# Performance work log

Hardware: AMD Instinct MI355X
Metric: run time of the kernel (lower is better)

## Reference

```python
import jax, jax.numpy as jnp
import numpy as np

B, LQ, LK, D = 16, 2048, 2048, 64
TEMPERATURE = 8.0  # sqrt(d_k)


def setup_inputs() -> dict:
    key = jax.random.key(0)
    kq, kk, kv, km = jax.random.split(key, 4)
    q = jax.random.normal(kq, (B, LQ, D), dtype=jnp.float32)
    k = jax.random.normal(kk, (B, LK, D), dtype=jnp.float32)
    v = jax.random.normal(kv, (B, LK, D), dtype=jnp.float32)
    mask = jax.random.randint(km, (B, LQ, LK), 0, 2).astype(jnp.bool_)
    return {"q": q, "k": k, "v": v, "mask": mask}


def reference(q, k, v, mask):
    # attn = bmm(q, k^T) / temperature  -> [B, LQ, LK]
    attn = jnp.einsum("bqd,bkd->bqk", q, k) / TEMPERATURE
    attn = jnp.where(mask, -jnp.inf, attn)
    attn = jax.nn.softmax(attn, axis=2)
    out = jnp.einsum("bqk,bkd->bqd", attn, v)  # [B, LQ, D]
    return out, attn
```

## Files before the change

### kernel.cpp

```cpp
#include <hip/hip_runtime.h>
#include <hip/hip_bf16.h>

namespace {
constexpr int kB = 16;
constexpr int kLQ = 2048;
constexpr int kLK = 2048;
constexpr int kD = 64;
constexpr float kLog2e = 1.44269504088896340736f;
constexpr int kQT = 64;
constexpr int kKT = 512;
constexpr int kKStrB = 144;
constexpr int kMStrB = 40;
constexpr int kBStrB = 72;
constexpr int kChunk = 256;
constexpr int kEStrB = 528;
}

using short8 = __attribute__((ext_vector_type(8))) short;
using f32x4 = __attribute__((ext_vector_type(4))) float;

union S8U { short8 v; unsigned u[4]; };

static __device__ __forceinline__ unsigned pk2(float lo, float hi) {
    __hip_bfloat162 h = __float22bfloat162_rn(float2{lo, hi});
    unsigned short a = __builtin_bit_cast(unsigned short, h.x);
    unsigned short b = __builtin_bit_cast(unsigned short, h.y);
    return (unsigned)a | ((unsigned)b << 16);
}
static __device__ __forceinline__ float bf2f(unsigned short s) {
    unsigned u = ((unsigned)s) << 16;
    return __builtin_bit_cast(float, u);
}

__global__ __launch_bounds__(256, 8) void k1_qke(
    const float* __restrict__ qg, const float* __restrict__ kg,
    const void* __restrict__ maskg, unsigned short* __restrict__ ews,
    float* __restrict__ outg)
{
    __shared__ __align__(16) unsigned char s_kst[32 * kKStrB];
    __shared__ __align__(16) unsigned char s_mst[64 * kMStrB];
    __shared__ __align__(16) unsigned char s_bnc[4][16 * kBStrB];
    __shared__ int s_flag;

    const int tid = threadIdx.x;
    const int wave = tid >> 6;
    const int lane = tid & 63;
    const int r16 = lane & 15;
    const int g = lane >> 4;

    const int blk = blockIdx.x;
    const int b = blk >> 7;
    const int kt = (blk >> 5) & 3;
    const int qt = blk & 31;
    const int rows0 = qt * kQT;
    const int c0 = kt * kKT;

    if (tid < 64) {
        unsigned w = ((const unsigned*)maskg)[tid];
        unsigned long long bal = __ballot((w & 0xFFFFFF00u) != 0u);
        if (tid == 0) s_flag = (bal != 0ull) ? 1 : 0;
    }
    __syncthreads();
    const bool mask_byte = (s_flag != 0);
    const unsigned char* mask_u8 = (const unsigned char*)maskg;
    const int* mask_i32 = (const int*)maskg;

    short8 q0, q1;
    {
        const float4* qp = (const float4*)(qg + ((size_t)b * kLQ + rows0 + wave * 16 + r16) * kD);
        const float s = 0.125f * kLog2e;
        float4 x0 = qp[2*g + 0], x1 = qp[2*g + 1];
        float4 x2 = qp[2*g + 8], x3 = qp[2*g + 9];
        x0 *= s; x1 *= s; x2 *= s; x3 *= s;
        S8U a, c;
        a.u[0] = pk2(x0.x, x0.y); a.u[1] = pk2(x0.z, x0.w);
        a.u[2] = pk2(x1.x, x1.y); a.u[3] = pk2(x1.z, x1.w);
        c.u[0] = pk2(x2.x, x2.y); c.u[1] = pk2(x2.z, x2.w);
        c.u[2] = pk2(x3.x, x3.y); c.u[3] = pk2(x3.z, x3.w);
        q0 = a.v; q1 = c.v;
    }

    float wsum = 0.f;

    for (int sub = 0; sub < kKT / 32; ++sub) {
        const int csub = c0 + sub * 32;
        {
            const int krow = tid >> 3;
            const int d8 = (tid & 7) * 8;
            const float4* kp = (const float4*)(kg + ((size_t)b * kLK + csub + krow) * kD + d8);
            float4 y0 = kp[0], y1 = kp[1];
            S8U p;
            p.u[0] = pk2(y0.x, y0.y); p.u[1] = pk2(y0.z, y0.w);
            p.u[2] = pk2(y1.x, y1.y); p.u[3] = pk2(y1.z, y1.w);
            *(short8*)(s_kst + krow * kKStrB + d8 * 2) = p.v;
        }
        {
            const int mrow = tid >> 2;
            const int mc = (tid & 3) * 8;
            unsigned long long f;
            if (mask_byte) {
                f = *(const unsigned long long*)(mask_u8 +
                        ((size_t)b * kLQ + rows0 + mrow) * (size_t)kLK + csub + mc);
            } else {
                const int* mp = mask_i32 + ((size_t)b * kLQ + rows0 + mrow) * (size_t)kLK + csub + mc;
                const int4 m0 = *(const int4*)mp;
                const int4 m1 = *(const int4*)(mp + 4);
                f  = (m0.x ? 1ull : 0ull)       | (m0.y ? 1ull << 8 : 0ull)
                   | (m0.z ? 1ull << 16 : 0ull) | (m0.w ? 1ull << 24 : 0ull)
                   | (m1.x ? 1ull << 32 : 0ull) | (m1.y ? 1ull << 40 : 0ull)
                   | (m1.z ? 1ull << 48 : 0ull) | (m1.w ? 1ull << 56 : 0ull);
            }
            *(unsigned long long*)(s_mst + mrow * kMStrB + mc) = f;
        }
        __syncthreads();

        const short8 kA0 = *(const short8*)(s_kst + r16 * kKStrB + g * 16);
        const short8 kA1 = *(const short8*)(s_kst + r16 * kKStrB + 64 + g * 16);
        const short8 kB0 = *(const short8*)(s_kst + (16 + r16) * kKStrB + g * 16);
        const short8 kB1 = *(const short8*)(s_kst + (16 + r16) * kKStrB + 64 + g * 16);
        f32x4 accA = {0.f, 0.f, 0.f, 0.f}, accB = {0.f, 0.f, 0.f, 0.f};
        accA = __builtin_amdgcn_mfma_f32_16x16x32_bf16(kA0, q0, accA, 0, 0, 0);
        accA = __builtin_amdgcn_mfma_f32_16x16x32_bf16(kA1, q1, accA, 0, 0, 0);
        accB = __builtin_amdgcn_mfma_f32_16x16x32_bf16(kB0, q0, accB, 0, 0, 0);
        accB = __builtin_amdgcn_mfma_f32_16x16x32_bf16(kB1, q1, accB, 0, 0, 0);

        const unsigned mwA = *(const unsigned*)(s_mst + (wave * 16 + r16) * kMStrB + 4 * g);
        const unsigned mwB = *(const unsigned*)(s_mst + (wave * 16 + r16) * kMStrB + 16 + 4 * g);
        float eA[4], eB[4];
#pragma unroll
        for (int r = 0; r < 4; ++r) {
            eA[r] = ((mwA >> (8*r)) & 0xFFu) ? 0.f : __builtin_amdgcn_exp2f(accA[r]);
            eB[r] = ((mwB >> (8*r)) & 0xFFu) ? 0.f : __builtin_amdgcn_exp2f(accB[r]);
        }
        wsum += (eA[0] + eA[1]) + (eA[2] + eA[3]) + (eB[0] + eB[1]) + (eB[2] + eB[3]);
        uint2 pA{ pk2(eA[0], eA[1]), pk2(eA[2], eA[3]) };
        uint2 pB{ pk2(eB[0], eB[1]), pk2(eB[2], eB[3]) };
        *(uint2*)(s_bnc[wave] + r16 * kBStrB + 8 * g) = pA;
        *(uint2*)(s_bnc[wave] + r16 * kBStrB + 32 + 8 * g) = pB;
        __syncthreads();

        {
            const int row = tid >> 2;
            const int seg = tid & 3;
            const S8U* src = (const S8U*)(s_bnc[row >> 4] + (row & 15) * kBStrB + seg * 16);
            unsigned short* dst = ews + ((size_t)b * kLQ + rows0 + row) * (size_t)kLK + csub + seg * 8;
            *(short8*)dst = src->v;
        }
    }
    wsum += __shfl_xor(wsum, 16, 64);
    wsum += __shfl_xor(wsum, 32, 64);
    if (g == 0)
        outg[((size_t)b * kLQ + rows0 + wave * 16 + r16) * kD + kt] = wsum;
}

__global__ __launch_bounds__(512, 8) void k2_norm_pv(
    const float* __restrict__ vg, const unsigned short* __restrict__ ews,
    float* __restrict__ attng, float* __restrict__ outg)
{
    __shared__ __align__(16) unsigned char s_e[16 * kEStrB];
    __shared__ float s_red[16][kD];
    __shared__ float s_rinv[16];

    const int tid = threadIdx.x;
    const int wave = tid >> 6;
    const int lane = tid & 63;
    const int r16 = lane & 15;
    const int g = lane >> 4;

    const int blk = blockIdx.x;
    const int b = blk >> 7;
    const int row0 = (blk & 127) * 16;

    if (tid < 64) {
        const int r = tid >> 2, p = tid & 3;
        float ps = outg[((size_t)b * kLQ + row0 + r) * kD + p];
        ps += __shfl_xor(ps, 1, 64);
        ps += __shfl_xor(ps, 2, 64);
        if (p == 0) s_rinv[r] = __builtin_amdgcn_rcpf(ps);
    }
    __syncthreads();

    const int d0 = (wave & 3) * 16;
    const int kh = wave >> 2;
    f32x4 acc = {0.f, 0.f, 0.f, 0.f};
    const float* vbase = vg + (size_t)b * kLK * kD + d0 + r16;

    for (int chunk = 0; chunk < kLK / kChunk; ++chunk) {
        const int c0 = chunk * kChunk;
        {
            const int row = tid >> 5;
            const int cc = tid & 31;
            const float rinv = s_rinv[row];
            const unsigned short* ep = ews + ((size_t)b * kLQ + row0 + row) * (size_t)kLK + c0 + cc * 8;
            const short8 ev = *(const short8*)ep;
            *(short8*)(s_e + row * kEStrB + cc * 16) = ev;
            float* ap = attng + ((size_t)b * kLQ + row0 + row) * (size_t)kLK + c0 + cc * 8;
            f32x4 a0, a1;
            a0[0] = bf2f((unsigned short)ev[0]) * rinv;
            a0[1] = bf2f((unsigned short)ev[1]) * rinv;
            a0[2] = bf2f((unsigned short)ev[2]) * rinv;
            a0[3] = bf2f((unsigned short)ev[3]) * rinv;
            a1[0] = bf2f((unsigned short)ev[4]) * rinv;
            a1[1] = bf2f((unsigned short)ev[5]) * rinv;
            a1[2] = bf2f((unsigned short)ev[6]) * rinv;
            a1[3] = bf2f((unsigned short)ev[7]) * rinv;
            *(f32x4*)ap = a0;
            *(f32x4*)(ap + 4) = a1;
        }
        __syncthreads();
#pragma unroll
        for (int s = 0; s < 4; ++s) {
            const int kk = kh * 128 + s * 32 + 8 * g;
            const short8 af = *(const short8*)(s_e + r16 * kEStrB + kk * 2);
            const float* vp = vbase + (size_t)(c0 + kk) * kD;
            float v0 = vp[0*kD], v1 = vp[1*kD], v2 = vp[2*kD], v3 = vp[3*kD];
            float v4 = vp[4*kD], v5 = vp[5*kD], v6 = vp[6*kD], v7 = vp[7*kD];
            S8U bv;
            bv.u[0] = pk2(v0, v1); bv.u[1] = pk2(v2, v3);
            bv.u[2] = pk2(v4, v5); bv.u[3] = pk2(v6, v7);
            acc = __builtin_amdgcn_mfma_f32_16x16x32_bf16(af, bv.v, acc, 0, 0, 0);
        }
        __syncthreads();
    }

    if (kh == 1) {
#pragma unroll
        for (int r = 0; r < 4; ++r) s_red[4*g + r][d0 + r16] = acc[r];
    }
    __syncthreads();
    if (kh == 0) {
#pragma unroll
        for (int r = 0; r < 4; ++r) {
            const int m = 4*g + r;
            outg[((size_t)b * kLQ + row0 + m) * kD + d0 + r16] =
                (acc[r] + s_red[m][d0 + r16]) * s_rinv[m];
        }
    }
}

extern "C" void kernel_launch(void* const* d_in, const int* in_sizes, int n_in,
                              void* d_out, int out_size, void* d_ws, size_t ws_size,
                              hipStream_t stream) {
    (void)in_sizes; (void)n_in; (void)out_size; (void)ws_size;
    const float* q = (const float*)d_in[0];
    const float* k = (const float*)d_in[1];
    const float* v = (const float*)d_in[2];
    const void* mask = d_in[3];
    float* out = (float*)d_out;
    float* attn = out + (size_t)kB * kLQ * kD;
    unsigned short* ews = (unsigned short*)d_ws;
    k1_qke<<<dim3(kB * 128), 256, 0, stream>>>(q, k, mask, ews, out);
    k2_norm_pv<<<dim3(kB * 128), 512, 0, stream>>>(v, ews, attn, out);
}
```

Baseline: 284.2 us.

## Give each k1 block full key rows and move attn normalization into k1

The first kernel now assigns each block 16 query rows across the full key length, with 128-key sub-tiles split across four waves. This lets the block compute complete row sums itself and write the normalized fp32 attention matrix, which previously happened in the second kernel. The second kernel is reduced to the P·V product using the stored reciprocal. The cost is that K is reloaded and converted by 128 blocks per batch instead of 32, and the exp workspace is read back right after being written (likely from L2). Occupancy also drops because the launch bound goes from 8 to 6 and LDS use is larger.

After: 288.3 us. About the same (+1.4%).

```diff
diff --git a/kernel.cpp b/kernel.cpp
--- a/kernel.cpp
+++ b/kernel.cpp
@@ -7,17 +7,15 @@
 constexpr int kLK = 2048;
 constexpr int kD = 64;
 constexpr float kLog2e = 1.44269504088896340736f;
-constexpr int kQT = 64;
-constexpr int kKT = 512;
 constexpr int kKStrB = 144;
-constexpr int kMStrB = 40;
-constexpr int kBStrB = 72;
+constexpr int kMStrB = 136;
+constexpr int kBStrB = 272;
 constexpr int kChunk = 256;
 constexpr int kEStrB = 528;
 }
 
 using short8 = __attribute__((ext_vector_type(8))) short;
-using f32x4 = __attribute__((ext_vector_type(4))) float;
+using f32x4  = __attribute__((ext_vector_type(4))) float;
 
 union S8U { short8 v; unsigned u[4]; };
 
@@ -32,14 +30,16 @@
     return __builtin_bit_cast(float, u);
 }
 
-__global__ __launch_bounds__(256, 8) void k1_qke(
+__global__ __launch_bounds__(256, 6) void k1_fused(
     const float* __restrict__ qg, const float* __restrict__ kg,
     const void* __restrict__ maskg, unsigned short* __restrict__ ews,
-    float* __restrict__ outg)
+    float* __restrict__ attng, float* __restrict__ outg)
 {
-    __shared__ __align__(16) unsigned char s_kst[32 * kKStrB];
-    __shared__ __align__(16) unsigned char s_mst[64 * kMStrB];
-    __shared__ __align__(16) unsigned char s_bnc[4][16 * kBStrB];
+    __shared__ __align__(16) unsigned char s_kst[128 * kKStrB];
+    __shared__ __align__(16) unsigned char s_mst[16 * kMStrB];
+    __shared__ __align__(16) unsigned char s_bnc[16 * kBStrB];
+    __shared__ float s_wsum[4][16];
+    __shared__ float s_rinv[16];
     __shared__ int s_flag;
 
     const int tid = threadIdx.x;
@@ -50,10 +50,8 @@
 
     const int blk = blockIdx.x;
     const int b = blk >> 7;
-    const int kt = (blk >> 5) & 3;
-    const int qt = blk & 31;
-    const int rows0 = qt * kQT;
-    const int c0 = kt * kKT;
+    const int qt = blk & 127;
+    const size_t grow0 = (size_t)b * kLQ + qt * 16;
 
     if (tid < 64) {
         unsigned w = ((const unsigned*)maskg)[tid];
@@ -67,7 +65,7 @@
 
     short8 q0, q1;
     {
-        const float4* qp = (const float4*)(qg + ((size_t)b * kLQ + rows0 + wave * 16 + r16) * kD);
+        const float4* qp = (const float4*)(qg + (grow0 + r16) * kD);
         const float s = 0.125f * kLog2e;
         float4 x0 = qp[2*g + 0], x1 = qp[2*g + 1];
         float4 x2 = qp[2*g + 8], x3 = qp[2*g + 9];
@@ -82,50 +80,47 @@
 
     float wsum = 0.f;
 
-    for (int sub = 0; sub < kKT / 32; ++sub) {
-        const int csub = c0 + sub * 32;
+    for (int sub = 0; sub < kLK / 128; ++sub) {
+        const int csub = sub * 128;
+#pragma unroll
+        for (int i = 0; i < 8; ++i) {
+            const int row = (tid >> 4) + i * 16;
+            const float4 y = *(const float4*)(kg + ((size_t)b * kLK + csub + row) * kD + (tid & 15) * 4);
+            uint2 p{ pk2(y.x, y.y), pk2(y.z, y.w) };
+            *(uint2*)(s_kst + row * kKStrB + (tid & 15) * 8) = p;
+        }
         {
-            const int krow = tid >> 3;
-            const int d8 = (tid & 7) * 8;
-            const float4* kp = (const float4*)(kg + ((size_t)b * kLK + csub + krow) * kD + d8);
-            float4 y0 = kp[0], y1 = kp[1];
-            S8U p;
-            p.u[0] = pk2(y0.x, y0.y); p.u[1] = pk2(y0.z, y0.w);
-            p.u[2] = pk2(y1.x, y1.y); p.u[3] = pk2(y1.z, y1.w);
-            *(short8*)(s_kst + krow * kKStrB + d8 * 2) = p.v;
-        }
-        {
-            const int mrow = tid >> 2;
-            const int mc = (tid & 3) * 8;
+            const int mrow = tid >> 4;
+            const int mseg = tid & 15;
             unsigned long long f;
             if (mask_byte) {
-                f = *(const unsigned long long*)(mask_u8 +
-                        ((size_t)b * kLQ + rows0 + mrow) * (size_t)kLK + csub + mc);
+                f = *(const unsigned long long*)(mask_u8 + (grow0 + mrow) * kLK + csub + mseg * 8);
             } else {
-                const int* mp = mask_i32 + ((size_t)b * kLQ + rows0 + mrow) * (size_t)kLK + csub + mc;
+                const int* mp = mask_i32 + (grow0 + mrow) * kLK + csub + mseg * 8;
                 const int4 m0 = *(const int4*)mp;
                 const int4 m1 = *(const int4*)(mp + 4);
-                f  = (m0.x ? 1ull : 0ull)       | (m0.y ? 1ull << 8 : 0ull)
-                   | (m0.z ? 1ull << 16 : 0ull) | (m0.w ? 1ull << 24 : 0ull)
-                   | (m1.x ? 1ull << 32 : 0ull) | (m1.y ? 1ull << 40 : 0ull)
-                   | (m1.z ? 1ull << 48 : 0ull) | (m1.w ? 1ull << 56 : 0ull);
+                f  = (m0.x ? 1ull : 0ull)        | (m0.y ? 1ull << 8 : 0ull)
+                   | (m0.z ? 1ull << 16 : 0ull)  | (m0.w ? 1ull << 24 : 0ull)
+                   | (m1.x ? 1ull << 32 : 0ull)  | (m1.y ? 1ull << 40 : 0ull)
+                   | (m1.z ? 1ull << 48 : 0ull)  | (m1.w ? 1ull << 56 : 0ull);
             }
-            *(unsigned long long*)(s_mst + mrow * kMStrB + mc) = f;
-        }
-        __syncthreads();
-
-        const short8 kA0 = *(const short8*)(s_kst + r16 * kKStrB + g * 16);
-        const short8 kA1 = *(const short8*)(s_kst + r16 * kKStrB + 64 + g * 16);
-        const short8 kB0 = *(const short8*)(s_kst + (16 + r16) * kKStrB + g * 16);
-        const short8 kB1 = *(const short8*)(s_kst + (16 + r16) * kKStrB + 64 + g * 16);
+            *(unsigned long long*)(s_mst + mrow * kMStrB + mseg * 8) = f;
+        }
+        __syncthreads();
+
+        const unsigned char* kb = s_kst + (wave * 32 + r16) * kKStrB;
+        const short8 kA0 = *(const short8*)(kb + g * 16);
+        const short8 kA1 = *(const short8*)(kb + 64 + g * 16);
+        const short8 kB0 = *(const short8*)(kb + 16 * kKStrB + g * 16);
+        const short8 kB1 = *(const short8*)(kb + 16 * kKStrB + 64 + g * 16);
         f32x4 accA = {0.f, 0.f, 0.f, 0.f}, accB = {0.f, 0.f, 0.f, 0.f};
         accA = __builtin_amdgcn_mfma_f32_16x16x32_bf16(kA0, q0, accA, 0, 0, 0);
         accA = __builtin_amdgcn_mfma_f32_16x16x32_bf16(kA1, q1, accA, 0, 0, 0);
         accB = __builtin_amdgcn_mfma_f32_16x16x32_bf16(kB0, q0, accB, 0, 0, 0);
         accB = __builtin_amdgcn_mfma_f32_16x16x32_bf16(kB1, q1, accB, 0, 0, 0);
 
-        const unsigned mwA = *(const unsigned*)(s_mst + (wave * 16 + r16) * kMStrB + 4 * g);
-        const unsigned mwB = *(const unsigned*)(s_mst + (wave * 16 + r16) * kMStrB + 16 + 4 * g);
+        const unsigned mwA = *(const unsigned*)(s_mst + r16 * kMStrB + wave * 32 + 4 * g);
+        const unsigned mwB = *(const unsigned*)(s_mst + r16 * kMStrB + wave * 32 + 16 + 4 * g);
         float eA[4], eB[4];
 #pragma unroll
         for (int r = 0; r < 4; ++r) {
@@ -135,27 +130,51 @@
         wsum += (eA[0] + eA[1]) + (eA[2] + eA[3]) + (eB[0] + eB[1]) + (eB[2] + eB[3]);
         uint2 pA{ pk2(eA[0], eA[1]), pk2(eA[2], eA[3]) };
         uint2 pB{ pk2(eB[0], eB[1]), pk2(eB[2], eB[3]) };
-        *(uint2*)(s_bnc[wave] + r16 * kBStrB + 8 * g) = pA;
-        *(uint2*)(s_bnc[wave] + r16 * kBStrB + 32 + 8 * g) = pB;
+        *(uint2*)(s_bnc + r16 * kBStrB + wave * 64 + 8 * g) = pA;
+        *(uint2*)(s_bnc + r16 * kBStrB + wave * 64 + 32 + 8 * g) = pB;
         __syncthreads();
 
         {
-            const int row = tid >> 2;
-            const int seg = tid & 3;
-            const S8U* src = (const S8U*)(s_bnc[row >> 4] + (row & 15) * kBStrB + seg * 16);
-            unsigned short* dst = ews + ((size_t)b * kLQ + rows0 + row) * (size_t)kLK + csub + seg * 8;
-            *(short8*)dst = src->v;
-        }
-    }
+            const int erow = tid >> 4;
+            const int eseg = tid & 15;
+            *(short8*)(ews + (grow0 + erow) * kLK + csub + eseg * 8) =
+                *(const short8*)(s_bnc + erow * kBStrB + eseg * 16);
+        }
+    }
+
     wsum += __shfl_xor(wsum, 16, 64);
     wsum += __shfl_xor(wsum, 32, 64);
-    if (g == 0)
-        outg[((size_t)b * kLQ + rows0 + wave * 16 + r16) * kD + kt] = wsum;
-}
-
-__global__ __launch_bounds__(512, 8) void k2_norm_pv(
+    if (g == 0) s_wsum[wave][r16] = wsum;
+    __syncthreads();
+    if (tid < 16) {
+        const float rs = s_wsum[0][tid] + s_wsum[1][tid] + s_wsum[2][tid] + s_wsum[3][tid];
+        outg[(grow0 + tid) * kD] = rs;
+        s_rinv[tid] = __builtin_amdgcn_rcpf(rs);
+    }
+    __syncthreads();
+
+#pragma unroll 2
+    for (int r = 0; r < 16; ++r) {
+        const float rinv = s_rinv[r];
+        const short8 ev = *(const short8*)(ews + (grow0 + r) * kLK + tid * 8);
+        f32x4 a0, a1;
+        a0[0] = bf2f((unsigned short)ev[0]) * rinv;
+        a0[1] = bf2f((unsigned short)ev[1]) * rinv;
+        a0[2] = bf2f((unsigned short)ev[2]) * rinv;
+        a0[3] = bf2f((unsigned short)ev[3]) * rinv;
+        a1[0] = bf2f((unsigned short)ev[4]) * rinv;
+        a1[1] = bf2f((unsigned short)ev[5]) * rinv;
+        a1[2] = bf2f((unsigned short)ev[6]) * rinv;
+        a1[3] = bf2f((unsigned short)ev[7]) * rinv;
+        float* ap = attng + (grow0 + r) * kLK + tid * 8;
+        *(f32x4*)ap = a0;
+        *(f32x4*)(ap + 4) = a1;
+    }
+}
+
+__global__ __launch_bounds__(512, 8) void k2_pv(
     const float* __restrict__ vg, const unsigned short* __restrict__ ews,
-    float* __restrict__ attng, float* __restrict__ outg)
+    float* __restrict__ outg)
 {
     __shared__ __align__(16) unsigned char s_e[16 * kEStrB];
     __shared__ float s_red[16][kD];
@@ -169,15 +188,10 @@
 
     const int blk = blockIdx.x;
     const int b = blk >> 7;
-    const int row0 = (blk & 127) * 16;
-
-    if (tid < 64) {
-        const int r = tid >> 2, p = tid & 3;
-        float ps = outg[((size_t)b * kLQ + row0 + r) * kD + p];
-        ps += __shfl_xor(ps, 1, 64);
-        ps += __shfl_xor(ps, 2, 64);
-        if (p == 0) s_rinv[r] = __builtin_amdgcn_rcpf(ps);
-    }
+    const size_t grow0 = (size_t)b * kLQ + (blk & 127) * 16;
+
+    if (tid < 16)
+        s_rinv[tid] = __builtin_amdgcn_rcpf(outg[(grow0 + tid) * kD]);
     __syncthreads();
 
     const int d0 = (wave & 3) * 16;
@@ -190,22 +204,8 @@
         {
             const int row = tid >> 5;
             const int cc = tid & 31;
-            const float rinv = s_rinv[row];
-            const unsigned short* ep = ews + ((size_t)b * kLQ + row0 + row) * (size_t)kLK + c0 + cc * 8;
-            const short8 ev = *(const short8*)ep;
+            const short8 ev = *(const short8*)(ews + (grow0 + row) * kLK + c0 + cc * 8);
             *(short8*)(s_e + row * kEStrB + cc * 16) = ev;
-            float* ap = attng + ((size_t)b * kLQ + row0 + row) * (size_t)kLK + c0 + cc * 8;
-            f32x4 a0, a1;
-            a0[0] = bf2f((unsigned short)ev[0]) * rinv;
-            a0[1] = bf2f((unsigned short)ev[1]) * rinv;
-            a0[2] = bf2f((unsigned short)ev[2]) * rinv;
-            a0[3] = bf2f((unsigned short)ev[3]) * rinv;
-            a1[0] = bf2f((unsigned short)ev[4]) * rinv;
-            a1[1] = bf2f((unsigned short)ev[5]) * rinv;
-            a1[2] = bf2f((unsigned short)ev[6]) * rinv;
-            a1[3] = bf2f((unsigned short)ev[7]) * rinv;
-            *(f32x4*)ap = a0;
-            *(f32x4*)(ap + 4) = a1;
         }
         __syncthreads();
 #pragma unroll
@@ -232,8 +232,7 @@
 #pragma unroll
         for (int r = 0; r < 4; ++r) {
             const int m = 4*g + r;
-            outg[((size_t)b * kLQ + row0 + m) * kD + d0 + r16] =
-                (acc[r] + s_red[m][d0 + r16]) * s_rinv[m];
+            outg[(grow0 + m) * kD + d0 + r16] = (acc[r] + s_red[m][d0 + r16]) * s_rinv[m];
         }
     }
 }
@@ -249,6 +248,6 @@
     float* out = (float*)d_out;
     float* attn = out + (size_t)kB * kLQ * kD;
     unsigned short* ews = (unsigned short*)d_ws;
-    k1_qke<<<dim3(kB * 128), 256, 0, stream>>>(q, k, mask, ews, out);
-    k2_norm_pv<<<dim3(kB * 128), 512, 0, stream>>>(v, ews, attn, out);
-}
+    k1_fused<<<dim3(kB * 128), 256, 0, stream>>>(q, k, mask, ews, attn, out);
+    k2_pv<<<dim3(kB * 128), 512, 0, stream>>>(v, ews, out);
+}
```
